# Performance work log

Measured on AMD Instinct MI355X. Metric: run time of the kernel, lower is better.

The kernel has to match this reference:

```python
import jax, jax.numpy as jnp
import numpy as np

D_MODEL = 256
N_HEADS = 8
N_LEVELS = 4
N_POINTS = 4
DH = D_MODEL // N_HEADS
SHAPES = [(100, 150), (50, 75), (25, 38), (13, 19)]  # per-level (H, W)
BATCH = 2


def setup_inputs() -> dict:
    key = jax.random.key(0)
    ks = jax.random.split(key, 8)
    Lq = sum(h * w for h, w in SHAPES)  # 19947
    d = D_MODEL
    off_dim = N_HEADS * N_LEVELS * N_POINTS * 2
    aw_dim = N_HEADS * N_LEVELS * N_POINTS
    s = 1.0 / np.sqrt(d).astype(np.float32)
    lsi = np.concatenate([[0], np.cumsum([h * w for h, w in SHAPES])[:-1]])
    return {
        "query": jax.random.normal(ks[0], (BATCH, Lq, d), jnp.float32),
        "reference_points": jax.random.uniform(ks[1], (BATCH, Lq, N_LEVELS, 2), jnp.float32),
        "input_flatten": jax.random.normal(ks[2], (BATCH, Lq, d), jnp.float32),
        "input_spatial_shapes": jnp.array(SHAPES, dtype=jnp.int32),
        "input_level_start_index": jnp.array(lsi, dtype=jnp.int32),
        "W_samp": 0.01 * jax.random.normal(ks[3], (off_dim, d), jnp.float32),
        "b_samp": 0.1 * jax.random.normal(ks[4], (off_dim,), jnp.float32),
        "W_attn": s * jax.random.normal(ks[5], (aw_dim, d), jnp.float32),
        "b_attn": jnp.zeros((aw_dim,), jnp.float32),
        "W_val": s * jax.random.normal(ks[6], (d, d), jnp.float32),
        "b_val": jnp.zeros((d,), jnp.float32),
        "W_out": s * jax.random.normal(ks[7], (d, d), jnp.float32),
        "b_out": jnp.zeros((d,), jnp.float32),
    }


def _bilinear(v, grid, Hl, Wl):
    # v: [N, H, Hl*Wl, Dh] flattened level feature map per head
    # grid: [N, H, Q, P, 2] in [-1, 1]; align_corners=False, zero padding
    N, H, Q, P, _ = grid.shape
    Dh = v.shape[-1]
    x = (grid[..., 0] + 1.0) * 0.5 * Wl - 0.5
    y = (grid[..., 1] + 1.0) * 0.5 * Hl - 0.5
    x0 = jnp.floor(x)
    y0 = jnp.floor(y)
    lx = x - x0
    ly = y - y0
    x0i = x0.astype(jnp.int32)
    y0i = y0.astype(jnp.int32)

    def corner(xi, yi, w):
        valid = (xi >= 0) & (xi < Wl) & (yi >= 0) & (yi < Hl)
        idx = jnp.clip(yi, 0, Hl - 1) * Wl + jnp.clip(xi, 0, Wl - 1)
        g = jnp.take_along_axis(v, idx.reshape(N, H, Q * P, 1), axis=2)
        return g.reshape(N, H, Q, P, Dh) * (w * valid)[..., None]

    return (corner(x0i, y0i, (1 - lx) * (1 - ly))
            + corner(x0i + 1, y0i, lx * (1 - ly))
            + corner(x0i, y0i + 1, (1 - lx) * ly)
            + corner(x0i + 1, y0i + 1, lx * ly))


def _forward(query, ref, x, shapes, W_samp, b_samp, W_attn, b_attn, W_val, b_val, W_out, b_out):
    N, Lq, d = query.shape
    H, L, P, Dh = N_HEADS, N_LEVELS, N_POINTS, DH
    # value projection -> [N, H, S, Dh]
    value = (x @ W_val.T + b_val).reshape(N, -1, H, Dh).transpose(0, 2, 1, 3)
    off = (query @ W_samp.T + b_samp).reshape(N, Lq, H, L, P, 2)
    attw = jax.nn.softmax((query @ W_attn.T + b_attn).reshape(N, Lq, H, L * P), axis=-1)
    attw = attw.reshape(N, Lq, H, L, P).transpose(0, 2, 1, 3, 4)  # [N,H,Lq,L,P]
    # offset normalizer is (W, H) per level
    norm = jnp.array([[w, h] for h, w in shapes], dtype=query.dtype)  # [L, 2]
    loc = ref[:, :, None, :, None, :] + off / norm[None, None, None, :, None, :]
    grids = (2.0 * loc - 1.0).transpose(0, 2, 1, 3, 4, 5)  # [N,H,Lq,L,P,2]

    acc = jnp.zeros((N, Lq, H, Dh), query.dtype)
    start = 0
    for lvl, (Hl, Wl) in enumerate(shapes):
        v = value[:, :, start:start + Hl * Wl]  # [N,H,Hl*Wl,Dh]
        start += Hl * Wl
        samp = _bilinear(v, grids[:, :, :, lvl], Hl, Wl)  # [N,H,Lq,P,Dh]
        acc = acc + jnp.einsum('nhqpd,nhqp->nqhd', samp, attw[:, :, :, lvl])
    out = acc.reshape(N, Lq, H * Dh)
    return out @ W_out.T + b_out


def reference(query, reference_points, input_flatten, input_spatial_shapes,
              input_level_start_index, W_samp, b_samp, W_attn, b_attn,
              W_val, b_val, W_out, b_out):
    shapes = [(int(h), int(w)) for h, w in np.asarray(input_spatial_shapes)]
    return _forward(query, reference_points, input_flatten, shapes,
                    W_samp, b_samp, W_attn, b_attn, W_val, b_val, W_out, b_out)
```

## Files before the change

kernel.cpp:

```cpp
#include <hip/hip_runtime.h>
#include <hip/hip_bf16.h>

#define NB 2
#define LQ 19947
#define LV 19947
#define DM 256
#define NH 8
#define NL 4
#define NP 4
#define MROWS (NB*LQ)
#define MPAD  39936
#define QPB 4

__device__ __constant__ int c_lvlH[4] = {100, 50, 25, 13};
__device__ __constant__ int c_lvlW[4] = {150, 75, 38, 19};
__device__ __constant__ int c_lvlS[4] = {0, 15000, 18750, 19700};

typedef __attribute__((ext_vector_type(8))) short short8;
typedef __attribute__((ext_vector_type(4))) float f32x4;

__device__ __forceinline__ unsigned short f2bf(float f) {
  unsigned u = __float_as_uint(f);
  u += 0x7FFFu + ((u >> 16) & 1u);
  return (unsigned short)(u >> 16);
}
__device__ __forceinline__ float bfl(unsigned u) { return __uint_as_float(u << 16); }
__device__ __forceinline__ float bfh(unsigned u) { return __uint_as_float(u & 0xFFFF0000u); }

__global__ __launch_bounds__(256) void f2b(
    const float* __restrict__ src, unsigned short* __restrict__ dst,
    int n_src, int n_dst)
{
  const int i = (blockIdx.x * 256 + threadIdx.x) * 4;
  if (i >= n_dst) return;
  ushort4 o;
  if (i + 4 <= n_src) {
    const float4 v = *(const float4*)(src + i);
    o.x = f2bf(v.x); o.y = f2bf(v.y); o.z = f2bf(v.z); o.w = f2bf(v.w);
  } else {
    float vs[4];
    #pragma unroll
    for (int j = 0; j < 4; ++j) vs[j] = (i + j < n_src) ? src[i + j] : 0.f;
    o.x = f2bf(vs[0]); o.y = f2bf(vs[1]); o.z = f2bf(vs[2]); o.w = f2bf(vs[3]);
  }
  *(ushort4*)(dst + i) = o;
}

__global__ __launch_bounds__(256) void wconv(
    const float* __restrict__ Wv, const float* __restrict__ Wsamp,
    const float* __restrict__ Wattn, const float* __restrict__ Wout,
    const float* __restrict__ bsamp, const float* __restrict__ battn,
    unsigned short* __restrict__ wvb, unsigned short* __restrict__ wqb,
    unsigned short* __restrict__ wob, float* __restrict__ bsa)
{
  const int b = blockIdx.x, t = threadIdx.x;
  if (b == 224) {
    if (t < 256) bsa[t] = bsamp[t];
    if (t < 128) bsa[256 + t] = battn[t];
    return;
  }
  const float* src; unsigned short* dst; int i;
  if (b < 64)       { src = Wv;    dst = wvb;          i = (b * 256 + t) * 4; }
  else if (b < 128) { src = Wsamp; dst = wqb;          i = ((b - 64) * 256 + t) * 4; }
  else if (b < 160) { src = Wattn; dst = wqb + 65536;  i = ((b - 128) * 256 + t) * 4; }
  else              { src = Wout;  dst = wob;          i = ((b - 160) * 256 + t) * 4; }
  const float4 v = *(const float4*)(src + i);
  ushort4 o;
  o.x = f2bf(v.x); o.y = f2bf(v.y); o.z = f2bf(v.z); o.w = f2bf(v.w);
  *(ushort4*)(dst + i) = o;
}

template<int OUT_BF16>
__global__ __launch_bounds__(256) void gemm_mfma(
    const unsigned short* __restrict__ Ab,
    const unsigned short* __restrict__ Wb,
    const float* __restrict__ bias,
    void* __restrict__ Cp,
    int Nn, int Mstore)
{
  __shared__ alignas(16) short As[128 * 32];
  __shared__ alignas(16) short Bs[128 * 32];

  const int t = threadIdx.x;
  const int w = t >> 6, l = t & 63;
  const int wr = w >> 1, wc = w & 1;
  const size_t rowBase = (size_t)blockIdx.x * 128;
  const int colBase = blockIdx.y * 128;

  const f32x4 z = {0.f, 0.f, 0.f, 0.f};
  f32x4 acc[4][4];
  #pragma unroll
  for (int i = 0; i < 4; ++i)
    #pragma unroll
    for (int j = 0; j < 4; ++j) acc[i][j] = z;

  const int srow = l >> 2;
  const int scol = (l & 3) * 8;

  for (int ks = 0; ks < 8; ++ks) {
    const int k0 = ks * 32;
    #pragma unroll
    for (int i = 0; i < 2; ++i) {
      const int ii = w * 2 + i;
      const unsigned short* gA = Ab + (rowBase + ii * 16 + srow) * 256 + k0 + scol;
      __builtin_amdgcn_global_load_lds(
          (const __attribute__((address_space(1))) void*)gA,
          (__attribute__((address_space(3))) void*)&As[ii * 512], 16, 0, 0);
      const unsigned short* gB = Wb + ((size_t)(colBase + ii * 16 + srow)) * 256 + k0 + scol;
      __builtin_amdgcn_global_load_lds(
          (const __attribute__((address_space(1))) void*)gB,
          (__attribute__((address_space(3))) void*)&Bs[ii * 512], 16, 0, 0);
    }
    __syncthreads();
    short8 af[4], bf[4];
    #pragma unroll
    for (int i = 0; i < 4; ++i) {
      af[i] = *(const short8*)&As[(wr * 64 + i * 16 + (l & 15)) * 32 + (l >> 4) * 8];
      bf[i] = *(const short8*)&Bs[(wc * 64 + i * 16 + (l & 15)) * 32 + (l >> 4) * 8];
    }
    #pragma unroll
    for (int i = 0; i < 4; ++i)
      #pragma unroll
      for (int j = 0; j < 4; ++j)
        acc[i][j] = __builtin_amdgcn_mfma_f32_16x16x32_bf16(bf[j], af[i], acc[i][j], 0, 0, 0);
    __syncthreads();
  }

  const int row0 = (int)rowBase + wr * 64 + (l & 15);
  const int col0 = colBase + wc * 64 + (l >> 4) * 4;
  #pragma unroll
  for (int j = 0; j < 4; ++j) {
    const float4 bj = *(const float4*)(bias + col0 + j * 16);
    #pragma unroll
    for (int i = 0; i < 4; ++i) {
      const int row = row0 + i * 16;
      if (row < Mstore) {
        const float v0 = acc[i][j][0] + bj.x;
        const float v1 = acc[i][j][1] + bj.y;
        const float v2 = acc[i][j][2] + bj.z;
        const float v3 = acc[i][j][3] + bj.w;
        if (OUT_BF16) {
          uint2 st;
          st.x = (unsigned)f2bf(v0) | ((unsigned)f2bf(v1) << 16);
          st.y = (unsigned)f2bf(v2) | ((unsigned)f2bf(v3) << 16);
          *(uint2*)((unsigned short*)Cp + (size_t)row * Nn + col0 + j * 16) = st;
        } else {
          *(float4*)((float*)Cp + (size_t)row * Nn + col0 + j * 16) =
              make_float4(v0, v1, v2, v3);
        }
      }
    }
  }
}

__global__ __launch_bounds__(256) void msda_sample(
    const unsigned short* __restrict__ value,
    const float* __restrict__ refp,
    const unsigned short* __restrict__ oc,
    unsigned short* __restrict__ accb)
{
  __shared__ float s_off[QPB][256];
  __shared__ float s_aw[QPB][128];
  __shared__ float s_ref[QPB][8];
  __shared__ unsigned s_poff[QPB][NH][17][4];
  __shared__ float    s_pw[QPB][NH][17][4];

  const int t = threadIdx.x;
  const int bq0 = blockIdx.x * QPB;

  {
    const int q = t >> 6, i = t & 63;
    const int bq = bq0 + q;
    if (bq < MROWS) {
      const unsigned short* row = oc + (size_t)bq * 384;
      const uint2 p = *(const uint2*)(row + i * 4);
      s_off[q][i * 4 + 0] = bfl(p.x);
      s_off[q][i * 4 + 1] = bfh(p.x);
      s_off[q][i * 4 + 2] = bfl(p.y);
      s_off[q][i * 4 + 3] = bfh(p.y);
      const unsigned pw = *(const unsigned*)(row + 256 + i * 2);
      s_aw[q][i * 2 + 0] = bfl(pw);
      s_aw[q][i * 2 + 1] = bfh(pw);
    }
    if (t < QPB * 8) {
      const int q2 = t >> 3, j = t & 7;
      if (bq0 + q2 < MROWS) s_ref[q2][j] = refp[(size_t)(bq0 + q2) * 8 + j];
    }
  }
  __syncthreads();

  if (t < QPB * NH) {
    const int q = t >> 3, h = t & 7;
    if (bq0 + q < MROWS) {
      float* aw = &s_aw[q][h * 16];
      float m = aw[0];
      #pragma unroll
      for (int i = 1; i < 16; ++i) m = fmaxf(m, aw[i]);
      float e[16]; float s = 0.f;
      #pragma unroll
      for (int i = 0; i < 16; ++i) { e[i] = __expf(aw[i] - m); s += e[i]; }
      const float inv = 1.f / s;
      #pragma unroll
      for (int i = 0; i < 16; ++i) aw[i] = e[i] * inv;
    }
  }
  __syncthreads();

  #pragma unroll
  for (int it = t; it < QPB * 128; it += 256) {
    const int q = it >> 7, rem = it & 127;
    const int h = rem >> 4, idx = rem & 15;
    const int l = idx >> 2;
    if (bq0 + q < MROWS) {
      const int Hl = c_lvlH[l], Wl = c_lvlW[l], st = c_lvlS[l];
      const float x = s_ref[q][l * 2 + 0] * (float)Wl - 0.5f + s_off[q][rem * 2 + 0];
      const float y = s_ref[q][l * 2 + 1] * (float)Hl - 0.5f + s_off[q][rem * 2 + 1];
      const float aw = s_aw[q][rem];
      const float x0f = floorf(x), y0f = floorf(y);
      const float lx = x - x0f, ly = y - y0f;
      const int x0 = (int)x0f, y0 = (int)y0f;
      const float vx0 = (x0 >= 0 && x0 < Wl) ? 1.f : 0.f;
      const float vx1 = (x0 >= -1 && x0 < Wl - 1) ? 1.f : 0.f;
      const float vy0 = (y0 >= 0 && y0 < Hl) ? 1.f : 0.f;
      const float vy1 = (y0 >= -1 && y0 < Hl - 1) ? 1.f : 0.f;
      const int xc0 = min(max(x0, 0), Wl - 1);
      const int xc1 = min(max(x0 + 1, 0), Wl - 1);
      const int yc0 = min(max(y0, 0), Hl - 1);
      const int yc1 = min(max(y0 + 1, 0), Hl - 1);
      const int r0 = st + yc0 * Wl, r1 = st + yc1 * Wl;
      s_poff[q][h][idx][0] = (unsigned)(r0 + xc0) * 512u;
      s_poff[q][h][idx][1] = (unsigned)(r0 + xc1) * 512u;
      s_poff[q][h][idx][2] = (unsigned)(r1 + xc0) * 512u;
      s_poff[q][h][idx][3] = (unsigned)(r1 + xc1) * 512u;
      s_pw[q][h][idx][0] = (1.f - lx) * (1.f - ly) * aw * (vx0 * vy0);
      s_pw[q][h][idx][1] = lx * (1.f - ly) * aw * (vx1 * vy0);
      s_pw[q][h][idx][2] = (1.f - lx) * ly * aw * (vx0 * vy1);
      s_pw[q][h][idx][3] = lx * ly * aw * (vx1 * vy1);
    }
  }
  __syncthreads();

  const int w = t >> 6;
  const int lane = t & 63;
  const int bq = bq0 + w;
  if (bq >= MROWS) return;
  const int n = bq / LQ;
  const char* vbase = (const char*)value + (size_t)n * LV * 512;
  const int h = lane >> 3;
  const int laneoff = h * 64 + (lane & 7) * 8;

  float a0 = 0.f, a1 = 0.f, a2 = 0.f, a3 = 0.f;
  #pragma unroll
  for (int idx = 0; idx < 16; ++idx) {
    const uint4  of = *(const uint4*)&s_poff[w][h][idx][0];
    const float4 wt = *(const float4*)&s_pw[w][h][idx][0];
    const uint2 p00 = *(const uint2*)(vbase + (of.x + laneoff));
    const uint2 p10 = *(const uint2*)(vbase + (of.y + laneoff));
    const uint2 p01 = *(const uint2*)(vbase + (of.z + laneoff));
    const uint2 p11 = *(const uint2*)(vbase + (of.w + laneoff));
    a0 += wt.x * bfl(p00.x) + wt.y * bfl(p10.x) + wt.z * bfl(p01.x) + wt.w * bfl(p11.x);
    a1 += wt.x * bfh(p00.x) + wt.y * bfh(p10.x) + wt.z * bfh(p01.x) + wt.w * bfh(p11.x);
    a2 += wt.x * bfl(p00.y) + wt.y * bfl(p10.y) + wt.z * bfl(p01.y) + wt.w * bfl(p11.y);
    a3 += wt.x * bfh(p00.y) + wt.y * bfh(p10.y) + wt.z * bfh(p01.y) + wt.w * bfh(p11.y);
  }
  ushort4 o;
  o.x = f2bf(a0); o.y = f2bf(a1); o.z = f2bf(a2); o.w = f2bf(a3);
  *(ushort4*)(accb + (size_t)bq * 256 + lane * 4) = o;
}

extern "C" void kernel_launch(void* const* d_in, const int* in_sizes, int n_in,
                              void* d_out, int out_size, void* d_ws, size_t ws_size,
                              hipStream_t stream) {
  const float* query  = (const float*)d_in[0];
  const float* refp   = (const float*)d_in[1];
  const float* xin    = (const float*)d_in[2];
  const float* W_samp = (const float*)d_in[5];
  const float* b_samp = (const float*)d_in[6];
  const float* W_attn = (const float*)d_in[7];
  const float* b_attn = (const float*)d_in[8];
  const float* W_val  = (const float*)d_in[9];
  const float* b_val  = (const float*)d_in[10];
  const float* W_out  = (const float*)d_in[11];
  const float* b_out  = (const float*)d_in[12];
  float* out = (float*)d_out;
  (void)in_sizes; (void)n_in; (void)out_size; (void)ws_size;

  char* ws = (char*)d_ws;
  unsigned short* value = (unsigned short*)(ws);
  unsigned short* qb    = (unsigned short*)(ws + 20447232);
  unsigned short* xb    = (unsigned short*)(ws + 40894464);
  unsigned short* accb  = xb;
  unsigned short* oc    = (unsigned short*)(ws + 61341696);
  unsigned short* wvb   = (unsigned short*)(ws + 92012544);
  unsigned short* wqb   = (unsigned short*)(ws + 92143616);
  unsigned short* wob   = (unsigned short*)(ws + 92340224);
  float*          bsa   = (float*)(ws + 92471296);

  hipLaunchKernelGGL(f2b, dim3(9984), dim3(256), 0, stream, xin,   xb, MROWS*256, MPAD*256);
  hipLaunchKernelGGL(f2b, dim3(9984), dim3(256), 0, stream, query, qb, MROWS*256, MPAD*256);
  hipLaunchKernelGGL(wconv, dim3(225), dim3(256), 0, stream,
                     W_val, W_samp, W_attn, W_out, b_samp, b_attn, wvb, wqb, wob, bsa);

  hipLaunchKernelGGL(HIP_KERNEL_NAME(gemm_mfma<1>), dim3(312, 2), dim3(256), 0, stream,
                     xb, wvb, b_val, value, 256, MPAD);
  hipLaunchKernelGGL(HIP_KERNEL_NAME(gemm_mfma<1>), dim3(312, 3), dim3(256), 0, stream,
                     qb, wqb, bsa, oc, 384, MPAD);
  hipLaunchKernelGGL(msda_sample, dim3((MROWS + QPB - 1) / QPB), dim3(256), 0, stream,
                     value, refp, oc, accb);
  hipLaunchKernelGGL(HIP_KERNEL_NAME(gemm_mfma<0>), dim3(312, 2), dim3(256), 0, stream,
                     accb, wob, b_out, out, 256, MROWS);
}
```

Baseline: 298.8 us.

## Merge conversion and front GEMM launches, shrink sampling blocks to two queries

Fuses the three fp32-to-bf16 conversion kernels into one launch and the value and query-projection GEMMs into a single 2D grid, cutting the launch count from seven to four. The sampling kernel now uses 128-thread blocks handling two queries each. It reads sampling offsets straight from global memory instead of staging them in shared memory, and drops the bounds checks, which is valid because MROWS is even. This aims to cut launch gaps and shared-memory use and to raise occupancy, at the cost of more blocks and less reuse of staged data per block.

```diff
diff --git a/kernel.cpp b/kernel.cpp
--- a/kernel.cpp
+++ b/kernel.cpp
@@ -10,7 +10,7 @@
 #define NP 4
 #define MROWS (NB*LQ)
 #define MPAD  39936
-#define QPB 4
+#define QPB 2
 
 __device__ __constant__ int c_lvlH[4] = {100, 50, 25, 13};
 __device__ __constant__ int c_lvlW[4] = {150, 75, 38, 19};
@@ -27,57 +27,54 @@
 __device__ __forceinline__ float bfl(unsigned u) { return __uint_as_float(u << 16); }
 __device__ __forceinline__ float bfh(unsigned u) { return __uint_as_float(u & 0xFFFF0000u); }
 
-__global__ __launch_bounds__(256) void f2b(
-    const float* __restrict__ src, unsigned short* __restrict__ dst,
-    int n_src, int n_dst)
+#define CB_X 9984
+__global__ __launch_bounds__(256) void conv_all(
+    const float* __restrict__ xin, const float* __restrict__ query,
+    const float* __restrict__ Wv, const float* __restrict__ Wsamp,
+    const float* __restrict__ Wattn, const float* __restrict__ Wout,
+    const float* __restrict__ bsamp, const float* __restrict__ battn,
+    unsigned short* __restrict__ xb, unsigned short* __restrict__ qb,
+    unsigned short* __restrict__ wvb, unsigned short* __restrict__ wqb,
+    unsigned short* __restrict__ wob, float* __restrict__ bsa)
 {
-  const int i = (blockIdx.x * 256 + threadIdx.x) * 4;
-  if (i >= n_dst) return;
+  const int b = blockIdx.x, t = threadIdx.x;
+  if (b == 2 * CB_X + 224) {
+    bsa[t] = bsamp[t];
+    if (t < 128) bsa[256 + t] = battn[t];
+    return;
+  }
+  const float* src; unsigned short* dst; int base, ns;
+  if (b < CB_X)            { src = xin;   dst = xb;          base = b * 1024;                ns = MROWS * 256; }
+  else if (b < 2*CB_X)     { src = query; dst = qb;          base = (b - CB_X) * 1024;       ns = MROWS * 256; }
+  else if (b < 2*CB_X+64)  { src = Wv;    dst = wvb;         base = (b - 2*CB_X) * 1024;     ns = 65536; }
+  else if (b < 2*CB_X+128) { src = Wsamp; dst = wqb;         base = (b - 2*CB_X-64) * 1024;  ns = 65536; }
+  else if (b < 2*CB_X+160) { src = Wattn; dst = wqb + 65536; base = (b - 2*CB_X-128) * 1024; ns = 32768; }
+  else                     { src = Wout;  dst = wob;         base = (b - 2*CB_X-160) * 1024; ns = 65536; }
+  const int i = base + t * 4;
   ushort4 o;
-  if (i + 4 <= n_src) {
+  if (i + 4 <= ns) {
     const float4 v = *(const float4*)(src + i);
     o.x = f2bf(v.x); o.y = f2bf(v.y); o.z = f2bf(v.z); o.w = f2bf(v.w);
   } else {
     float vs[4];
     #pragma unroll
-    for (int j = 0; j < 4; ++j) vs[j] = (i + j < n_src) ? src[i + j] : 0.f;
+    for (int j = 0; j < 4; ++j) vs[j] = (i + j < ns) ? src[i + j] : 0.f;
     o.x = f2bf(vs[0]); o.y = f2bf(vs[1]); o.z = f2bf(vs[2]); o.w = f2bf(vs[3]);
   }
   *(ushort4*)(dst + i) = o;
 }
 
-__global__ __launch_bounds__(256) void wconv(
-    const float* __restrict__ Wv, const float* __restrict__ Wsamp,
-    const float* __restrict__ Wattn, const float* __restrict__ Wout,
-    const float* __restrict__ bsamp, const float* __restrict__ battn,
-    unsigned short* __restrict__ wvb, unsigned short* __restrict__ wqb,
-    unsigned short* __restrict__ wob, float* __restrict__ bsa)
+__global__ __launch_bounds__(256) void gemm_front(
+    const unsigned short* __restrict__ xb, const unsigned short* __restrict__ qb,
+    const unsigned short* __restrict__ wvb, const unsigned short* __restrict__ wqb,
+    const float* __restrict__ b_val, const float* __restrict__ bsa,
+    unsigned short* __restrict__ value, unsigned short* __restrict__ oc)
 {
-  const int b = blockIdx.x, t = threadIdx.x;
-  if (b == 224) {
-    if (t < 256) bsa[t] = bsamp[t];
-    if (t < 128) bsa[256 + t] = battn[t];
-    return;
-  }
-  const float* src; unsigned short* dst; int i;
-  if (b < 64)       { src = Wv;    dst = wvb;          i = (b * 256 + t) * 4; }
-  else if (b < 128) { src = Wsamp; dst = wqb;          i = ((b - 64) * 256 + t) * 4; }
-  else if (b < 160) { src = Wattn; dst = wqb + 65536;  i = ((b - 128) * 256 + t) * 4; }
-  else              { src = Wout;  dst = wob;          i = ((b - 160) * 256 + t) * 4; }
-  const float4 v = *(const float4*)(src + i);
-  ushort4 o;
-  o.x = f2bf(v.x); o.y = f2bf(v.y); o.z = f2bf(v.z); o.w = f2bf(v.w);
-  *(ushort4*)(dst + i) = o;
-}
-
-template<int OUT_BF16>
-__global__ __launch_bounds__(256) void gemm_mfma(
-    const unsigned short* __restrict__ Ab,
-    const unsigned short* __restrict__ Wb,
-    const float* __restrict__ bias,
-    void* __restrict__ Cp,
-    int Nn, int Mstore)
-{
+  const unsigned short* Ab; const unsigned short* Wb; const float* bias;
+  unsigned short* Cp; int Nn, cb;
+  if (blockIdx.y < 2) { Ab = xb; Wb = wvb; bias = b_val; Cp = value; Nn = 256; cb = blockIdx.y; }
+  else                { Ab = qb; Wb = wqb; bias = bsa;   Cp = oc;    Nn = 384; cb = blockIdx.y - 2; }
+
   __shared__ alignas(16) short As[128 * 32];
   __shared__ alignas(16) short Bs[128 * 32];
 
@@ -85,7 +82,7 @@
   const int w = t >> 6, l = t & 63;
   const int wr = w >> 1, wc = w & 1;
   const size_t rowBase = (size_t)blockIdx.x * 128;
-  const int colBase = blockIdx.y * 128;
+  const int colBase = cb * 128;
 
   const f32x4 z = {0.f, 0.f, 0.f, 0.f};
   f32x4 acc[4][4];
@@ -134,36 +131,93 @@
     #pragma unroll
     for (int i = 0; i < 4; ++i) {
       const int row = row0 + i * 16;
-      if (row < Mstore) {
-        const float v0 = acc[i][j][0] + bj.x;
-        const float v1 = acc[i][j][1] + bj.y;
-        const float v2 = acc[i][j][2] + bj.z;
-        const float v3 = acc[i][j][3] + bj.w;
-        if (OUT_BF16) {
-          uint2 st;
-          st.x = (unsigned)f2bf(v0) | ((unsigned)f2bf(v1) << 16);
-          st.y = (unsigned)f2bf(v2) | ((unsigned)f2bf(v3) << 16);
-          *(uint2*)((unsigned short*)Cp + (size_t)row * Nn + col0 + j * 16) = st;
-        } else {
-          *(float4*)((float*)Cp + (size_t)row * Nn + col0 + j * 16) =
-              make_float4(v0, v1, v2, v3);
-        }
+      uint2 st;
+      st.x = (unsigned)f2bf(acc[i][j][0] + bj.x) | ((unsigned)f2bf(acc[i][j][1] + bj.y) << 16);
+      st.y = (unsigned)f2bf(acc[i][j][2] + bj.z) | ((unsigned)f2bf(acc[i][j][3] + bj.w) << 16);
+      *(uint2*)(Cp + (size_t)row * Nn + col0 + j * 16) = st;
+    }
+  }
+}
+
+__global__ __launch_bounds__(256) void gemm_out(
+    const unsigned short* __restrict__ Ab, const unsigned short* __restrict__ Wb,
+    const float* __restrict__ bias, float* __restrict__ Cp)
+{
+  __shared__ alignas(16) short As[128 * 32];
+  __shared__ alignas(16) short Bs[128 * 32];
+
+  const int t = threadIdx.x;
+  const int w = t >> 6, l = t & 63;
+  const int wr = w >> 1, wc = w & 1;
+  const size_t rowBase = (size_t)blockIdx.x * 128;
+  const int colBase = blockIdx.y * 128;
+
+  const f32x4 z = {0.f, 0.f, 0.f, 0.f};
+  f32x4 acc[4][4];
+  #pragma unroll
+  for (int i = 0; i < 4; ++i)
+    #pragma unroll
+    for (int j = 0; j < 4; ++j) acc[i][j] = z;
+
+  const int srow = l >> 2;
+  const int scol = (l & 3) * 8;
+
+  for (int ks = 0; ks < 8; ++ks) {
+    const int k0 = ks * 32;
+    #pragma unroll
+    for (int i = 0; i < 2; ++i) {
+      const int ii = w * 2 + i;
+      const unsigned short* gA = Ab + (rowBase + ii * 16 + srow) * 256 + k0 + scol;
+      __builtin_amdgcn_global_load_lds(
+          (const __attribute__((address_space(1))) void*)gA,
+          (__attribute__((address_space(3))) void*)&As[ii * 512], 16, 0, 0);
+      const unsigned short* gB = Wb + ((size_t)(colBase + ii * 16 + srow)) * 256 + k0 + scol;
+      __builtin_amdgcn_global_load_lds(
+          (const __attribute__((address_space(1))) void*)gB,
+          (__attribute__((address_space(3))) void*)&Bs[ii * 512], 16, 0, 0);
+    }
+    __syncthreads();
+    short8 af[4], bf[4];
+    #pragma unroll
+    for (int i = 0; i < 4; ++i) {
+      af[i] = *(const short8*)&As[(wr * 64 + i * 16 + (l & 15)) * 32 + (l >> 4) * 8];
+      bf[i] = *(const short8*)&Bs[(wc * 64 + i * 16 + (l & 15)) * 32 + (l >> 4) * 8];
+    }
+    #pragma unroll
+    for (int i = 0; i < 4; ++i)
+      #pragma unroll
+      for (int j = 0; j < 4; ++j)
+        acc[i][j] = __builtin_amdgcn_mfma_f32_16x16x32_bf16(bf[j], af[i], acc[i][j], 0, 0, 0);
+    __syncthreads();
+  }
+
+  const int row0 = (int)rowBase + wr * 64 + (l & 15);
+  const int col0 = colBase + wc * 64 + (l >> 4) * 4;
+  #pragma unroll
+  for (int j = 0; j < 4; ++j) {
+    const float4 bj = *(const float4*)(bias + col0 + j * 16);
+    #pragma unroll
+    for (int i = 0; i < 4; ++i) {
+      const int row = row0 + i * 16;
+      if (row < MROWS) {
+        *(float4*)(Cp + (size_t)row * 256 + col0 + j * 16) =
+            make_float4(acc[i][j][0] + bj.x, acc[i][j][1] + bj.y,
+                        acc[i][j][2] + bj.z, acc[i][j][3] + bj.w);
       }
     }
   }
 }
 
-__global__ __launch_bounds__(256) void msda_sample(
+__global__ __launch_bounds__(128) void msda_sample(
     const unsigned short* __restrict__ value,
     const float* __restrict__ refp,
     const unsigned short* __restrict__ oc,
     unsigned short* __restrict__ accb)
 {
-  __shared__ float s_off[QPB][256];
   __shared__ float s_aw[QPB][128];
   __shared__ float s_ref[QPB][8];
-  __shared__ unsigned s_poff[QPB][NH][17][4];
-  __shared__ float    s_pw[QPB][NH][17][4];
+  __shared__ alignas(16) unsigned s_poff[QPB][NH][17][4];
+  __shared__ alignas(16) float    s_pw[QPB][NH][17][4];
 
   const int t = threadIdx.x;
   const int bq0 = blockIdx.x * QPB;
@@ -171,79 +225,68 @@
   {
     const int q = t >> 6, i = t & 63;
     const int bq = bq0 + q;
-    if (bq < MROWS) {
-      const unsigned short* row = oc + (size_t)bq * 384;
-      const uint2 p = *(const uint2*)(row + i * 4);
-      s_off[q][i * 4 + 0] = bfl(p.x);
-      s_off[q][i * 4 + 1] = bfh(p.x);
-      s_off[q][i * 4 + 2] = bfl(p.y);
-      s_off[q][i * 4 + 3] = bfh(p.y);
-      const unsigned pw = *(const unsigned*)(row + 256 + i * 2);
-      s_aw[q][i * 2 + 0] = bfl(pw);
-      s_aw[q][i * 2 + 1] = bfh(pw);
-    }
+    const unsigned pw = *(const unsigned*)(oc + (size_t)bq * 384 + 256 + i * 2);
+    s_aw[q][i * 2 + 0] = bfl(pw);
+    s_aw[q][i * 2 + 1] = bfh(pw);
     if (t < QPB * 8) {
       const int q2 = t >> 3, j = t & 7;
-      if (bq0 + q2 < MROWS) s_ref[q2][j] = refp[(size_t)(bq0 + q2) * 8 + j];
+      s_ref[q2][j] = refp[(size_t)(bq0 + q2) * 8 + j];
     }
   }
   __syncthreads();
 
   if (t < QPB * NH) {
     const int q = t >> 3, h = t & 7;
-    if (bq0 + q < MROWS) {
-      float* aw = &s_aw[q][h * 16];
-      float m = aw[0];
-      #pragma unroll
-      for (int i = 1; i < 16; ++i) m = fmaxf(m, aw[i]);
-      float e[16]; float s = 0.f;
-      #pragma unroll
-      for (int i = 0; i < 16; ++i) { e[i] = __expf(aw[i] - m); s += e[i]; }
-      const float inv = 1.f / s;
-      #pragma unroll
-      for (int i = 0; i < 16; ++i) aw[i] = e[i] * inv;
-    }
+    float* aw = &s_aw[q][h * 16];
+    float m = aw[0];
+    #pragma unroll
+    for (int i = 1; i < 16; ++i) m = fmaxf(m, aw[i]);
+    float e[16]; float s = 0.f;
+    #pragma unroll
+    for (int i = 0; i < 16; ++i) { e[i] = __expf(aw[i] - m); s += e[i]; }
+    const float inv = 1.f / s;
+    #pragma unroll
+    for (int i = 0; i < 16; ++i) aw[i] = e[i] * inv;
   }
   __syncthreads();
 
   #pragma unroll
-  for (int it = t; it < QPB * 128; it += 256) {
+  for (int it = t; it < QPB * 128; it += 128) {
     const int q = it >> 7, rem = it & 127;
     const int h = rem >> 4, idx = rem & 15;
     const int l = idx >> 2;
-    if (bq0 + q < MROWS) {
-      const int Hl = c_lvlH[l], Wl = c_lvlW[l], st = c_lvlS[l];
-      const float x = s_ref[q][l * 2 + 0] * (float)Wl - 0.5f + s_off[q][rem * 2 + 0];
-      const float y = s_ref[q][l * 2 + 1] * (float)Hl - 0.5f + s_off[q][rem * 2 + 1];
-      const float aw = s_aw[q][rem];
-      const float x0f = floorf(x), y0f = floorf(y);
-      const float lx = x - x0f, ly = y - y0f;
-      const int x0 = (int)x0f, y0 = (int)y0f;
-      const float vx0 = (x0 >= 0 && x0 < Wl) ? 1.f : 0.f;
-      const float vx1 = (x0 >= -1 && x0 < Wl - 1) ? 1.f : 0.f;
-      const float vy0 = (y0 >= 0 && y0 < Hl) ? 1.f : 0.f;
-      const float vy1 = (y0 >= -1 && y0 < Hl - 1) ? 1.f : 0.f;
-      const int xc0 = min(max(x0, 0), Wl - 1);
-      const int xc1 = min(max(x0 + 1, 0), Wl - 1);
-      const int yc0 = min(max(y0, 0), Hl - 1);
-      const int yc1 = min(max(y0 + 1, 0), Hl - 1);
-      const int r0 = st + yc0 * Wl, r1 = st + yc1 * Wl;
-      s_poff[q][h][idx][0] = (unsigned)(r0 + xc0) * 512u;
-      s_poff[q][h][idx][1] = (unsigned)(r0 + xc1) * 512u;
-      s_poff[q][h][idx][2] = (unsigned)(r1 + xc0) * 512u;
-      s_poff[q][h][idx][3] = (unsigned)(r1 + xc1) * 512u;
-      s_pw[q][h][idx][0] = (1.f - lx) * (1.f - ly) * aw * (vx0 * vy0);
-      s_pw[q][h][idx][1] = lx * (1.f - ly) * aw * (vx1 * vy0);
-      s_pw[q][h][idx][2] = (1.f - lx) * ly * aw * (vx0 * vy1);
-      s_pw[q][h][idx][3] = lx * ly * aw * (vx1 * vy1);
-    }
+    const int bq = bq0 + q;
+    const unsigned po = *(const unsigned*)(oc + (size_t)bq * 384 + rem * 2);
+    const int Hl = c_lvlH[l], Wl = c_lvlW[l], st = c_lvlS[l];
+    const float x = s_ref[q][l * 2 + 0] * (float)Wl - 0.5f + bfl(po);
+    const float y = s_ref[q][l * 2 + 1] * (float)Hl - 0.5f + bfh(po);
+    const float aw = s_aw[q][rem];
+    const float x0f = floorf(x), y0f = floorf(y);
+    const float lx = x - x0f, ly = y - y0f;
+    const int x0 = (int)x0f, y0 = (int)y0f;
+    const float vx0 = (x0 >= 0 && x0 < Wl) ? 1.f : 0.f;
+    const float vx1 = (x0 >= -1 && x0 < Wl - 1) ? 1.f : 0.f;
+    const float vy0 = (y0 >= 0 && y0 < Hl) ? 1.f : 0.f;
+    const float vy1 = (y0 >= -1 && y0 < Hl - 1) ? 1.f : 0.f;
+    const int xc0 = min(max(x0, 0), Wl - 1);
+    const int xc1 = min(max(x0 + 1, 0), Wl - 1);
+    const int yc0 = min(max(y0, 0), Hl - 1);
+    const int yc1 = min(max(y0 + 1, 0), Hl - 1);
+    const int r0 = st + yc0 * Wl, r1 = st + yc1 * Wl;
+    s_poff[q][h][idx][0] = (unsigned)(r0 + xc0) * 512u;
+    s_poff[q][h][idx][1] = (unsigned)(r0 + xc1) * 512u;
+    s_poff[q][h][idx][2] = (unsigned)(r1 + xc0) * 512u;
+    s_poff[q][h][idx][3] = (unsigned)(r1 + xc1) * 512u;
+    s_pw[q][h][idx][0] = (1.f - lx) * (1.f - ly) * aw * (vx0 * vy0);
+    s_pw[q][h][idx][1] = lx * (1.f - ly) * aw * (vx1 * vy0);
+    s_pw[q][h][idx][2] = (1.f - lx) * ly * aw * (vx0 * vy1);
+    s_pw[q][h][idx][3] = lx * ly * aw * (vx1 * vy1);
   }
   __syncthreads();
 
   const int w = t >> 6;
   const int lane = t & 63;
   const int bq = bq0 + w;
-  if (bq >= MROWS) return;
   const int n = bq / LQ;
   const char* vbase = (const char*)value + (size_t)n * LV * 512;
   const int h = lane >> 3;
@@ -296,17 +339,13 @@
   unsigned short* wob   = (unsigned short*)(ws + 92340224);
   float*          bsa   = (float*)(ws + 92471296);
 
-  hipLaunchKernelGGL(f2b, dim3(9984), dim3(256), 0, stream, xin,   xb, MROWS*256, MPAD*256);
-  hipLaunchKernelGGL(f2b, dim3(9984), dim3(256), 0, stream, query, qb, MROWS*256, MPAD*256);
-  hipLaunchKernelGGL(wconv, dim3(225), dim3(256), 0, stream,
-                     W_val, W_samp, W_attn, W_out, b_samp, b_attn, wvb, wqb, wob, bsa);
-
-  hipLaunchKernelGGL(HIP_KERNEL_NAME(gemm_mfma<1>), dim3(312, 2), dim3(256), 0, stream,
-                     xb, wvb, b_val, value, 256, MPAD);
-  hipLaunchKernelGGL(HIP_KERNEL_NAME(gemm_mfma<1>), dim3(312, 3), dim3(256), 0, stream,
-                     qb, wqb, bsa, oc, 384, MPAD);
-  hipLaunchKernelGGL(msda_sample, dim3((MROWS + QPB - 1) / QPB), dim3(256), 0, stream,
+  hipLaunchKernelGGL(conv_all, dim3(2 * CB_X + 225), dim3(256), 0, stream,
+                     xin, query, W_val, W_samp, W_attn, W_out, b_samp, b_attn,
+                     xb, qb, wvb, wqb, wob, bsa);
+  hipLaunchKernelGGL(gemm_front, dim3(312, 5), dim3(256), 0, stream,
+                     xb, qb, wvb, wqb, b_val, bsa, value, oc);
+  hipLaunchKernelGGL(msda_sample, dim3(MROWS / QPB), dim3(128), 0, stream,
                      value, refp, oc, accb);
-  hipLaunchKernelGGL(HIP_KERNEL_NAME(gemm_mfma<0>), dim3(312, 2), dim3(256), 0, stream,
-                     accb, wob, b_out, out, 256, MROWS);
-}
+  hipLaunchKernelGGL(gemm_out, dim3(312, 2), dim3(256), 0, stream,
+                     accb, wob, b_out, out);
+}
```

New measurement: 281.5 us. 1.06x faster.
